# Kernel optimization log

Measured on AMD Instinct MI355X. Metric: run time of the kernel, lower is better.

The kernel has to match this reference:

```python
import jax, jax.numpy as jnp
import numpy as np

M, N, E, ES, D = 50000, 20000, 200000, 100000, 256

def _ln(x, g, b, eps=1e-5):
    mu = jnp.mean(x, -1, keepdims=True)
    var = jnp.mean((x - mu) ** 2, -1, keepdims=True)
    return (x - mu) * jax.lax.rsqrt(var + eps) * g + b

def _bn_train(x, g, b, eps=1e-5):
    # BatchNorm1d forward in training mode: batch statistics over rows
    mu = jnp.mean(x, 0)
    var = jnp.mean((x - mu) ** 2, 0)
    return (x - mu) * jax.lax.rsqrt(var + eps) * g + b

def _encoder(x, source, Wq, Wk, Wv, Wm, bm, ln1_g, ln1_b, mw1, mb1, mw2, mb2, ln2_g, ln2_b):
    # LoFTR-style linear-attention cross encoder, nhead=1
    Q = jax.nn.elu(x @ Wq) + 1.0          # [L,D]
    K = jax.nn.elu(source @ Wk) + 1.0     # [S,D]
    V = source @ Wv                        # [S,D]
    KV = K.T @ V                           # [D,D]
    Z = Q @ jnp.sum(K, 0) + 1e-6           # [L]
    msg = (Q @ KV) / Z[:, None]            # [L,D]
    msg = _ln(msg @ Wm + bm, ln1_g, ln1_b)
    y = jnp.concatenate([x, msg], -1)      # [L,2D]
    y = jax.nn.relu(y @ mw1 + mb1) @ mw2 + mb2
    return x + _ln(y, ln2_g, ln2_b)

def setup_inputs() -> dict:
    key = jax.random.key(0)
    ks = jax.random.split(key, 20)
    s = 1.0 / np.sqrt(D)
    s2 = 1.0 / np.sqrt(2 * D)
    inp = {
        'h_nodes': jax.random.normal(ks[0], (M, D), jnp.float32),
        's_u': jax.random.normal(ks[1], (N, D), jnp.float32),
        'g_src': jax.random.randint(ks[2], (E,), 0, M, jnp.int32),
        'g_dst': jax.random.randint(ks[3], (E,), 0, M, jnp.int32),
        's_src': jax.random.randint(ks[4], (ES,), 0, N, jnp.int32),
        's_dst': jax.random.randint(ks[5], (ES,), 0, N, jnp.int32),
        'conv_w': jax.random.normal(ks[6], (1, 2, 3), jnp.float32) * 0.3,
        'conv_b': jnp.zeros((1,), jnp.float32),
        'W2': jax.random.normal(ks[7], (D, D), jnp.float32) * s,
        'b2': jnp.zeros((D,), jnp.float32),
        'W4': jax.random.normal(ks[8], (D, D), jnp.float32) * s,
        'b4': jnp.zeros((D,), jnp.float32),
        'bn_g': jnp.ones((D,), jnp.float32),
        'bn_b': jnp.zeros((D,), jnp.float32),
        'Wq': jax.random.normal(ks[9], (D, D), jnp.float32) * s,
        'Wk': jax.random.normal(ks[10], (D, D), jnp.float32) * s,
        'Wv': jax.random.normal(ks[11], (D, D), jnp.float32) * s,
        'Wm': jax.random.normal(ks[12], (D, D), jnp.float32) * s,
        'bm': jnp.zeros((D,), jnp.float32),
        'ln1_g': jnp.ones((D,), jnp.float32),
        'ln1_b': jnp.zeros((D,), jnp.float32),
        'mw1': jax.random.normal(ks[13], (2 * D, 2 * D), jnp.float32) * s2,
        'mb1': jnp.zeros((2 * D,), jnp.float32),
        'mw2': jax.random.normal(ks[14], (2 * D, D), jnp.float32) * s2,
        'mb2': jnp.zeros((D,), jnp.float32),
        'ln2_g': jnp.ones((D,), jnp.float32),
        'ln2_b': jnp.zeros((D,), jnp.float32),
    }
    return inp

def reference(h_nodes, s_u, g_src, g_dst, s_src, s_dst, conv_w, conv_b, W2, b2, W4, b4,
              bn_g, bn_b, Wq, Wk, Wv, Wm, bm, ln1_g, ln1_b, mw1, mb1, mw2, mb2, ln2_g, ln2_b):
    enc = lambda x, src: _encoder(x, src, Wq, Wk, Wv, Wm, bm, ln1_g, ln1_b,
                                  mw1, mb1, mw2, mb2, ln2_g, ln2_b)
    # --- local edge features: gather src/dst, Conv1d(2->1,k=3,p=1), Linear ---
    src = h_nodes[g_src]                         # [E,D]
    dst = h_nodes[g_dst]                         # [E,D]
    edge_in = jnp.stack([src, dst], 1)           # [E,2,D]
    xp = jnp.pad(edge_in, ((0, 0), (0, 0), (1, 1)))
    conv = conv_b[0]
    for c in range(2):
        for j in range(3):
            conv = conv + conv_w[0, c, j] * xp[:, c, j:j + D]
    lr_e_local = conv @ W2 + b2                  # [E,D]
    # --- CrossTransformer (shared encoder weights across HUR/UVR/UUR) ---
    x = enc(h_nodes[:N], s_u)                    # user refinement [N,D]
    h_n = h_nodes.at[:N].set(x)
    edge = enc(h_n[g_src], h_n[g_dst])           # [E,D]
    social_edge = enc(x[s_src], x[s_dst])        # [ES,D]
    # --- fuse + BN + ReLU (dropout off for deterministic reference) ---
    lr_e = edge @ W4 + b4 + lr_e_local
    lr_e = jax.nn.relu(_bn_train(lr_e, bn_g, bn_b))
    social_edge = _bn_train(social_edge, bn_g, bn_b)
    return (lr_e, social_edge)
```

## Files before the change

### kernel.cpp

```cpp
#include <hip/hip_runtime.h>

static constexpr int Mn  = 50000;
static constexpr int Nn  = 20000;
static constexpr int En  = 200000;
static constexpr int ESn = 100000;

typedef short short8v __attribute__((ext_vector_type(8)));
typedef short short4v __attribute__((ext_vector_type(4)));
typedef float f32x4   __attribute__((ext_vector_type(4)));

__device__ __forceinline__ float b2f(unsigned short h) {
  unsigned int u = ((unsigned int)h) << 16;
  return __builtin_bit_cast(float, u);
}
__device__ __forceinline__ unsigned short f2b(float f) {
  unsigned int u = __builtin_bit_cast(unsigned int, f);
  u = (u + 0x7FFFu + ((u >> 16) & 1u)) >> 16;
  return (unsigned short)u;
}
__device__ __forceinline__ void gld16(const void* g, void* l) {
  __builtin_amdgcn_global_load_lds(
      (const __attribute__((address_space(1))) void*)g,
      (__attribute__((address_space(3))) void*)l, 16, 0, 0);
}

__global__ __launch_bounds__(256) void cvt_b(const float* __restrict__ s,
                                             unsigned short* __restrict__ d, long n) {
  long g  = (long)blockIdx.x*256 + threadIdx.x;
  long st = (long)gridDim.x*256;
  for (; g*8 < n; g += st) {
    const float4 a = *(const float4*)(s + g*8);
    const float4 b = *(const float4*)(s + g*8 + 4);
    short8v o;
    o[0]=(short)f2b(a.x); o[1]=(short)f2b(a.y); o[2]=(short)f2b(a.z); o[3]=(short)f2b(a.w);
    o[4]=(short)f2b(b.x); o[5]=(short)f2b(b.y); o[6]=(short)f2b(b.z); o[7]=(short)f2b(b.w);
    *(short8v*)(d + g*8) = o;
  }
}

__global__ __launch_bounds__(128) void wp_build(const float* __restrict__ W, int K, int N,
    unsigned short* __restrict__ WP, int KKd, int kg0) {
  const int t = threadIdx.x;
  const int kk2 = t >> 6, l = t & 63;
  const int c16 = blockIdx.x, ky = blockIdx.y;
  const int k0 = ky*64 + kk2*32 + (l>>4)*8;
  const int n  = c16*16 + (l&15);
  short8v o;
#pragma unroll
  for (int e=0;e<8;++e) o[e] = (short)f2b(W[(long)(k0+e)*N + n]);
  *(short8v*)(WP + (((long)c16*KKd + kg0 + ky*2+kk2)*64 + l)*8) = o;
}

__global__ __launch_bounds__(256) void kvw_mul(const float* __restrict__ KV,
    const float* __restrict__ Wm, float* __restrict__ KVW) {
  const int a = blockIdx.x;
  const int c = threadIdx.x;
  float s = 0.f;
  for (int b = 0; b < 256; ++b) s += KV[a*256 + b] * Wm[(long)b*256 + c];
  KVW[a*256 + c] = s;
}

__global__ __launch_bounds__(256) void count_idx(const int* __restrict__ idx, int n,
                                                 int* __restrict__ cnt) {
  int i = blockIdx.x*256 + threadIdx.x;
  const int st = gridDim.x*256;
  for (; i < n; i += st) atomicAdd(&cnt[idx[i]], 1);
}

__global__ __launch_bounds__(256,3) void gemm_kv(
    const unsigned short* __restrict__ X, int aoff,
    const unsigned short* __restrict__ WkP, const unsigned short* __restrict__ WvP,
    unsigned short* __restrict__ KbT, unsigned short* __restrict__ VbT,
    float* __restrict__ pS, int ldp, int nrows, const int* __restrict__ cntw)
{
  __shared__ short xb[4][64*64];
  const int t = threadIdx.x;
  const int w = t >> 6, l = t & 63, q = l >> 4, hw = l & 15;
  const int r0 = blockIdx.x << 6;

  {
    const int sr = l >> 3, sc = l & 7;
    const int gcol = ((sc ^ sr) << 3);
#pragma unroll
    for (int j=0;j<2;++j) {
      int lr = r0 + j*32 + w*8 + sr;
      int lrc = lr < nrows ? lr : nrows-1;
      const unsigned short* src = X + (long)(aoff+lrc)*256 + gcol;
#pragma unroll
      for (int ks=0;ks<4;++ks)
        gld16(src + ks*64, &xb[ks][(j*32 + w*8)*64]);
    }
  }
  asm volatile("s_waitcnt vmcnt(0)" ::: "memory");
  __builtin_amdgcn_s_barrier();

#pragma unroll
  for (int pass=0; pass<2; ++pass) {
    const unsigned short* WP = pass ? WvP : WkP;
    unsigned short* O = pass ? VbT : KbT;
    f32x4 acc[4][4];
#pragma unroll
    for (int m=0;m<4;++m)
#pragma unroll
      for (int n=0;n<4;++n) acc[m][n] = (f32x4){0.f,0.f,0.f,0.f};
    short8v bfc[4], bfn[4];
#pragma unroll
    for (int n=0;n<4;++n)
      bfc[n] = *(const short8v*)(WP + (((long)(w*4+n)*8)*64 + l)*8);
#pragma unroll
    for (int st=0; st<8; ++st) {
      if (st < 7) {
#pragma unroll
        for (int n=0;n<4;++n)
          bfn[n] = *(const short8v*)(WP + (((long)(w*4+n)*8 + st+1)*64 + l)*8);
      }
      const int ks = st >> 1;
      const int kc = ((st&1)<<2) + q;
      short8v af[4];
#pragma unroll
      for (int m=0;m<4;++m)
        af[m] = *(const short8v*)&xb[ks][(m*16+hw)*64 + ((kc^(hw&7))<<3)];
      __builtin_amdgcn_s_setprio(1);
#pragma unroll
      for (int m=0;m<4;++m)
#pragma unroll
        for (int n=0;n<4;++n)
          acc[m][n] = __builtin_amdgcn_mfma_f32_16x16x32_bf16(af[m], bfc[n], acc[m][n], 0,0,0);
      __builtin_amdgcn_s_setprio(0);
#pragma unroll
      for (int n=0;n<4;++n) bfc[n] = bfn[n];
    }
    float colsum[4] = {0.f,0.f,0.f,0.f};
#pragma unroll
    for (int m=0;m<4;++m)
#pragma unroll
      for (int n=0;n<4;++n) {
        const int c = w*64 + n*16 + hw;
        short4v o4;
#pragma unroll
        for (int i=0;i<4;++i) {
          const int lr = r0 + m*16 + q*4 + i;
          float v = 0.f;
          if (lr < nrows) {
            v = acc[m][n][i];
            if (pass == 0) {
              v = v > 0.f ? v + 1.f : __expf(v);
              if (cntw) v *= (float)cntw[aoff + lr];
            }
          }
          if (pass == 0) colsum[n] += v;
          o4[i] = (short)f2b(v);
        }
        *(short4v*)(O + (long)c*ldp + r0 + m*16 + q*4) = o4;
      }
    if (pass == 0) {
#pragma unroll
      for (int n=0;n<4;++n) {
        float s = colsum[n];
        s += __shfl_xor(s, 16);
        s += __shfl_xor(s, 32);
        if (q == 0) pS[(long)blockIdx.x*256 + w*64 + n*16 + hw] = s;
      }
    }
  }
}

__global__ __launch_bounds__(256) void ksum_red(const float* __restrict__ pS, int nb,
    float* __restrict__ Ks) {
  __shared__ float ws[4];
  const int c = blockIdx.x;
  const int t = threadIdx.x;
  float s = 0.f;
  for (int b = t; b < nb; b += 256) s += pS[(long)b*256 + c];
#pragma unroll
  for (int off=32; off; off>>=1) s += __shfl_xor(s, off);
  if ((t & 63) == 0) ws[t >> 6] = s;
  __syncthreads();
  if (t == 0) Ks[c] += ws[0] + ws[1] + ws[2] + ws[3];
}

__global__ __launch_bounds__(256,4) void ktv_mfma(
    const unsigned short* __restrict__ KbT, const unsigned short* __restrict__ VbT,
    int ldp, int rpp, float* __restrict__ pKV)
{
  const int t  = threadIdx.x;
  const int w  = t >> 6;
  const int l  = t & 63;
  const int q  = l >> 4;
  const int hw = l & 15;
  const int wa = w >> 1, wb = w & 1;
  const int a0 = blockIdx.x << 7;
  const int b0 = blockIdx.y << 7;
  const int rbeg = blockIdx.z * rpp;
  const int rend = min(ldp, rbeg + rpp);

  f32x4 acc[4][4];
#pragma unroll
  for (int m=0;m<4;++m)
#pragma unroll
    for (int n=0;n<4;++n) acc[m][n] = (f32x4){0.f,0.f,0.f,0.f};

  const unsigned short* ap[4];
  const unsigned short* bp[4];
#pragma unroll
  for (int m=0;m<4;++m) ap[m] = KbT + (long)(a0 + wa*64 + m*16 + hw)*ldp + q*8;
#pragma unroll
  for (int n=0;n<4;++n) bp[n] = VbT + (long)(b0 + wb*64 + n*16 + hw)*ldp + q*8;

#pragma unroll 4
  for (int r = rbeg; r < rend; r += 32) {
    short8v af[4], bf[4];
#pragma unroll
    for (int m=0;m<4;++m) af[m] = *(const short8v*)(ap[m] + r);
#pragma unroll
    for (int n=0;n<4;++n) bf[n] = *(const short8v*)(bp[n] + r);
#pragma unroll
    for (int m=0;m<4;++m)
#pragma unroll
      for (int n=0;n<4;++n)
        acc[m][n] = __builtin_amdgcn_mfma_f32_16x16x32_bf16(af[m], bf[n], acc[m][n], 0,0,0);
  }

  const long base = (long)blockIdx.z * 65536;
#pragma unroll
  for (int m=0;m<4;++m)
#pragma unroll
    for (int i=0;i<4;++i) {
      const int a = a0 + wa*64 + m*16 + q*4 + i;
#pragma unroll
      for (int n=0;n<4;++n) {
        const int b = b0 + wb*64 + n*16 + hw;
        pKV[base + (long)a*256 + b] = acc[m][n][i];
      }
    }
}

__global__ __launch_bounds__(256) void kv_accum(const float* __restrict__ pKV, int P,
                                                float* __restrict__ KV) {
  const int i = blockIdx.x*256 + threadIdx.x;
  float s = 0.f;
  for (int p=0;p<P;++p) s += pKV[(long)p*65536 + i];
  KV[i] += s;
}

template<int OMODE>
__global__ __launch_bounds__(256,2) void encB(
    const unsigned short* __restrict__ X, int aoff,
    const unsigned short* __restrict__ WqP, const unsigned short* __restrict__ KVWP,
    const unsigned short* __restrict__ m1P, const unsigned short* __restrict__ m2P,
    const float* __restrict__ Ksum, const float* __restrict__ bmv,
    const float* __restrict__ l1g, const float* __restrict__ l1b,
    const float* __restrict__ mb1, const float* __restrict__ mb2,
    const float* __restrict__ l2g, const float* __restrict__ l2b,
    const unsigned short* __restrict__ WfP,
    void* outv, int dc0, int nrows)
{
  __shared__ short xb[4][64*64];
  __shared__ short qb[4][64*64];
  __shared__ short y1b[64*64];
  __shared__ float2 red[64][4];
  __shared__ float Zl[64];

  const int t = threadIdx.x;
  const int w = t >> 6, l = t & 63, q = l >> 4, hw = l & 15;
  const int wc = w;
  const int r0 = blockIdx.x << 6;
  const int sr = l >> 3, sc = l & 7;
  const int gcol = ((sc ^ sr) << 3);

  {
#pragma unroll
    for (int j=0;j<2;++j) {
      int lr = r0 + j*32 + w*8 + sr;
      int lrc = lr < nrows ? lr : nrows-1;
      const unsigned short* src = X + (long)(aoff+lrc)*256 + gcol;
#pragma unroll
      for (int ks=0;ks<4;++ks)
        gld16(src + ks*64, &xb[ks][(j*32 + w*8)*64]);
    }
  }
  asm volatile("s_waitcnt vmcnt(0)" ::: "memory");
  __builtin_amdgcn_s_barrier();

  f32x4 acc[4][4];

  auto GEMM256 = [&](const short* Asrc, const unsigned short* WP) {
#pragma unroll
    for (int m=0;m<4;++m)
#pragma unroll
      for (int n=0;n<4;++n) acc[m][n] = (f32x4){0.f,0.f,0.f,0.f};
    short8v bfc[4], bfn[4];
#pragma unroll
    for (int n=0;n<4;++n)
      bfc[n] = *(const short8v*)(WP + (((long)(wc*4+n)*8)*64 + l)*8);
#pragma unroll
    for (int st=0; st<8; ++st) {
      if (st < 7) {
#pragma unroll
        for (int n=0;n<4;++n)
          bfn[n] = *(const short8v*)(WP + (((long)(wc*4+n)*8 + st+1)*64 + l)*8);
      }
      const int ks = st >> 1;
      const int kc = ((st&1)<<2) + q;
      short8v af[4];
#pragma unroll
      for (int m=0;m<4;++m)
        af[m] = *(const short8v*)&Asrc[ks*4096 + (m*16+hw)*64 + ((kc^(hw&7))<<3)];
      __builtin_amdgcn_s_setprio(1);
#pragma unroll
      for (int m=0;m<4;++m)
#pragma unroll
        for (int n=0;n<4;++n)
          acc[m][n] = __builtin_amdgcn_mfma_f32_16x16x32_bf16(af[m], bfc[n], acc[m][n], 0,0,0);
      __builtin_amdgcn_s_setprio(0);
#pragma unroll
      for (int n=0;n<4;++n) bfc[n] = bfn[n];
    }
  };

  GEMM256(&xb[0][0], WqP);
  {
    float ksv[4];
#pragma unroll
    for (int n=0;n<4;++n) ksv[n] = Ksum[wc*64+n*16+hw];
#pragma unroll
    for (int m=0;m<4;++m)
#pragma unroll
      for (int n=0;n<4;++n)
#pragma unroll
        for (int i=0;i<4;++i) {
          float v = acc[m][n][i];
          acc[m][n][i] = v > 0.f ? v + 1.f : __expf(v);
        }
#pragma unroll
    for (int m=0;m<4;++m)
#pragma unroll
      for (int i=0;i<4;++i) {
        float z = 0.f;
#pragma unroll
        for (int n=0;n<4;++n) z += acc[m][n][i]*ksv[n];
#pragma unroll
        for (int off=1; off<16; off<<=1) z += __shfl_xor(z, off);
        if (hw==0) red[m*16+q*4+i][wc] = make_float2(z, 0.f);
      }
#pragma unroll
    for (int m=0;m<4;++m)
#pragma unroll
      for (int i=0;i<4;++i) {
        const int row = m*16+q*4+i;
        const int sw = row & 7;
#pragma unroll
        for (int n=0;n<4;++n)
          qb[wc][row*64 + (((n*2+(hw>>3)) ^ sw)<<3) + (hw&7)] = (short)f2b(acc[m][n][i]);
      }
  }
  __syncthreads();
  if (wc==0 && hw==0) {
#pragma unroll
    for (int m=0;m<4;++m)
#pragma unroll
      for (int i=0;i<4;++i) {
        const int row = m*16+q*4+i;
        Zl[row] = red[row][0].x + red[row][1].x + red[row][2].x + red[row][3].x + 1e-6f;
      }
  }

  GEMM256(&qb[0][0], KVWP);
  __syncthreads();
#pragma unroll
  for (int m=0;m<4;++m) {
    const f32x4 z = *(const f32x4*)&Zl[m*16+q*4];
#pragma unroll
    for (int i=0;i<4;++i) {
      const float iz = 1.f / z[i];
#pragma unroll
      for (int n=0;n<4;++n) acc[m][n][i] *= iz;
    }
  }
  {
    float lg[4], lb[4];
#pragma unroll
    for (int n=0;n<4;++n) {
      const int c = wc*64+n*16+hw;
      const float bv = bmv[c];
      lg[n] = l1g[c]; lb[n] = l1b[c];
#pragma unroll
      for (int m=0;m<4;++m)
#pragma unroll
        for (int i=0;i<4;++i) acc[m][n][i] += bv;
    }
    float s1[4][4], s2[4][4];
#pragma unroll
    for (int m=0;m<4;++m)
#pragma unroll
      for (int i=0;i<4;++i) {
        float s=0.f, sq=0.f;
#pragma unroll
        for (int n=0;n<4;++n){ const float v=acc[m][n][i]; s+=v; sq+=v*v; }
        s1[m][i]=s; s2[m][i]=sq;
      }
#pragma unroll
    for (int off=1; off<16; off<<=1)
#pragma unroll
      for (int m=0;m<4;++m)
#pragma unroll
        for (int i=0;i<4;++i) {
          s1[m][i] += __shfl_xor(s1[m][i], off);
          s2[m][i] += __shfl_xor(s2[m][i], off);
        }
    if (hw==0) {
#pragma unroll
      for (int m=0;m<4;++m)
#pragma unroll
        for (int i=0;i<4;++i)
          red[m*16+q*4+i][wc] = make_float2(s1[m][i], s2[m][i]);
    }
    __syncthreads();
#pragma unroll
    for (int m=0;m<4;++m)
#pragma unroll
      for (int i=0;i<4;++i) {
        const int row = m*16+q*4+i;
        float ts=0.f, tq=0.f;
#pragma unroll
        for (int ww=0;ww<4;++ww){ const float2 v=red[row][ww]; ts+=v.x; tq+=v.y; }
        const float mmu = ts*(1.f/256.f);
        float var = tq*(1.f/256.f) - mmu*mmu;
        var = var>0.f ? var : 0.f;
        const float rs = rsqrtf(var + 1e-5f);
        const int sw = row & 7;
#pragma unroll
        for (int n=0;n<4;++n) {
          const float v = (acc[m][n][i]-mmu)*rs*lg[n] + lb[n];
          qb[wc][row*64 + (((n*2+(hw>>3)) ^ sw)<<3) + (hw&7)] = (short)f2b(v);
        }
      }
  }
  __syncthreads();

  f32x4 oacc[4][4];
#pragma unroll
  for (int m=0;m<4;++m)
#pragma unroll
    for (int n=0;n<4;++n) oacc[m][n] = (f32x4){0.f,0.f,0.f,0.f};

  for (int ct=0; ct<8; ++ct) {
    f32x4 ya[4];
#pragma unroll
    for (int m=0;m<4;++m) ya[m] = (f32x4){0.f,0.f,0.f,0.f};
    {
      short8v b0c, b0n;
      b0c = *(const short8v*)(m1P + (((long)(ct*4+wc)*16)*64 + l)*8);
#pragma unroll
      for (int st=0; st<16; ++st) {
        if (st < 15)
          b0n = *(const short8v*)(m1P + (((long)(ct*4+wc)*16 + st+1)*64 + l)*8);
        const int ks = st >> 1;
        const int kc = ((st&1)<<2) + q;
        const short* As_ = (ks<4) ? &xb[ks][0] : &qb[ks-4][0];
        __builtin_amdgcn_s_setprio(1);
#pragma unroll
        for (int m=0;m<4;++m) {
          const short8v af = *(const short8v*)&As_[(m*16+hw)*64 + ((kc^(hw&7))<<3)];
          ya[m] = __builtin_amdgcn_mfma_f32_16x16x32_bf16(af, b0c, ya[m], 0,0,0);
        }
        __builtin_amdgcn_s_setprio(0);
        b0c = b0n;
      }
    }
    const float b1 = mb1[ct*64 + wc*16 + hw];
#pragma unroll
    for (int m=0;m<4;++m)
#pragma unroll
      for (int i=0;i<4;++i) {
        const int row = m*16+q*4+i;
        float v = ya[m][i] + b1; v = v>0.f ? v : 0.f;
        y1b[row*64 + (((wc*2+(hw>>3)) ^ (row&7))<<3) + (hw&7)] = (short)f2b(v);
      }
    __syncthreads();
    {
      short8v bfc[4], bfn[4];
#pragma unroll
      for (int n=0;n<4;++n)
        bfc[n] = *(const short8v*)(m2P + (((long)(wc*4+n)*16 + ct*2)*64 + l)*8);
#pragma unroll
      for (int kk=0;kk<2;++kk) {
        if (kk == 0) {
#pragma unroll
          for (int n=0;n<4;++n)
            bfn[n] = *(const short8v*)(m2P + (((long)(wc*4+n)*16 + ct*2+1)*64 + l)*8);
        }
        const int kc = (kk<<2)+q;
        short8v af[4];
#pragma unroll
        for (int m=0;m<4;++m)
          af[m] = *(const short8v*)&y1b[(m*16+hw)*64 + ((kc^(hw&7))<<3)];
        __builtin_amdgcn_s_setprio(1);
#pragma unroll
        for (int m=0;m<4;++m)
#pragma unroll
          for (int n=0;n<4;++n)
            oacc[m][n] = __builtin_amdgcn_mfma_f32_16x16x32_bf16(af[m], bfc[n], oacc[m][n], 0,0,0);
        __builtin_amdgcn_s_setprio(0);
#pragma unroll
        for (int n=0;n<4;++n) bfc[n] = bfn[n];
      }
    }
    __syncthreads();
  }

  {
    float lg[4], lb[4];
#pragma unroll
    for (int n=0;n<4;++n) {
      const int c = wc*64+n*16+hw;
      const float bv = mb2[c];
      lg[n] = l2g[c]; lb[n] = l2b[c];
#pragma unroll
      for (int m=0;m<4;++m)
#pragma unroll
        for (int i=0;i<4;++i) oacc[m][n][i] += bv;
    }
    float s1[4][4], s2[4][4];
#pragma unroll
    for (int m=0;m<4;++m)
#pragma unroll
      for (int i=0;i<4;++i) {
        float s=0.f, sq=0.f;
#pragma unroll
        for (int n=0;n<4;++n){ const float v=oacc[m][n][i]; s+=v; sq+=v*v; }
        s1[m][i]=s; s2[m][i]=sq;
      }
#pragma unroll
    for (int off=1; off<16; off<<=1)
#pragma unroll
      for (int m=0;m<4;++m)
#pragma unroll
        for (int i=0;i<4;++i) {
          s1[m][i] += __shfl_xor(s1[m][i], off);
          s2[m][i] += __shfl_xor(s2[m][i], off);
        }
    if (hw==0) {
#pragma unroll
      for (int m=0;m<4;++m)
#pragma unroll
        for (int i=0;i<4;++i)
          red[m*16+q*4+i][wc] = make_float2(s1[m][i], s2[m][i]);
    }
    __syncthreads();
#pragma unroll
    for (int m=0;m<4;++m)
#pragma unroll
      for (int i=0;i<4;++i) {
        const int row = m*16+q*4+i;
        const int lr = r0 + row;
        if (lr >= nrows) continue;
        float ts=0.f, tq=0.f;
#pragma unroll
        for (int ww=0;ww<4;++ww){ const float2 v=red[row][ww]; ts+=v.x; tq+=v.y; }
        const float mmu = ts*(1.f/256.f);
        float var = tq*(1.f/256.f) - mmu*mmu;
        var = var>0.f ? var : 0.f;
        const float rs = rsqrtf(var + 1e-5f);
        const int sw = row & 7;
#pragma unroll
        for (int n=0;n<4;++n) {
          const int c = wc*64+n*16+hw;
          float v = (oacc[m][n][i]-mmu)*rs*lg[n] + lb[n];
          v += b2f((unsigned short)xb[wc][row*64 + (((n*2+(hw>>3)) ^ sw)<<3) + (hw&7)]);
          if constexpr (OMODE == 2) {
            qb[wc][row*64 + (((n*2+(hw>>3)) ^ sw)<<3) + (hw&7)] = (short)f2b(v);
          } else {
            const long off2 = (long)(dc0+lr)*256 + c;
            if constexpr (OMODE == 1) ((float*)outv)[off2] = v;
            else ((unsigned short*)outv)[off2] = f2b(v);
          }
        }
      }
  }

  if constexpr (OMODE == 2) {
    __syncthreads();
    GEMM256(&qb[0][0], WfP);
#pragma unroll
    for (int m=0;m<4;++m)
#pragma unroll
      for (int i=0;i<4;++i) {
        const int lr = r0 + m*16 + q*4 + i;
        if (lr >= nrows) continue;
#pragma unroll
        for (int n=0;n<4;++n)
          ((float*)outv)[(long)(dc0+lr)*256 + wc*64+n*16+hw] = acc[m][n][i];
      }
  }
}

__global__ __launch_bounds__(256,3) void edge_final(
    const float* __restrict__ h, const int* __restrict__ gs, const int* __restrict__ gd,
    const float* __restrict__ cw, const float* __restrict__ cb,
    const unsigned short* __restrict__ W2P, const float* __restrict__ EW4,
    const float* __restrict__ b4, const float* __restrict__ b2,
    float* __restrict__ lr_e, int nrows)
{
  __shared__ short xb[4][64*64];
  const int t = threadIdx.x;
  const int w = t >> 6, l = t & 63, q = l >> 4, hw = l & 15;
  const int r0 = blockIdx.x << 6;

  const float c0=cw[0],c1=cw[1],c2=cw[2],c3=cw[3],c4=cw[4],c5=cw[5],cbb=cb[0];
  for (int it=0; it<16; ++it) {
    const int row = w*16 + it;
    const int lr = r0 + row;
    const int lrc = lr < nrows ? lr : nrows-1;
    const float4 s = *(const float4*)(h + (long)gs[lrc]*256 + l*4);
    const float4 d = *(const float4*)(h + (long)gd[lrc]*256 + l*4);
    float smw = __shfl_up(s.w, 1); if (l==0) smw = 0.f;
    float spx = __shfl_down(s.x, 1); if (l==63) spx = 0.f;
    float dmw = __shfl_up(d.w, 1); if (l==0) dmw = 0.f;
    float dpx = __shfl_down(d.x, 1); if (l==63) dpx = 0.f;
    short4v o;
    o[0]=(short)f2b(cbb + c0*smw + c1*s.x + c2*s.y + c3*dmw + c4*d.x + c5*d.y);
    o[1]=(short)f2b(cbb + c0*s.x + c1*s.y + c2*s.z + c3*d.x + c4*d.y + c5*d.z);
    o[2]=(short)f2b(cbb + c0*s.y + c1*s.z + c2*s.w + c3*d.y + c4*d.z + c5*d.w);
    o[3]=(short)f2b(cbb + c0*s.z + c1*s.w + c2*spx + c3*d.z + c4*d.w + c5*dpx);
    const int ks = l >> 4;
    const int g  = (l & 15) >> 1;
    *(short4v*)&xb[ks][row*64 + ((g ^ (row&7))<<3) + (l&1)*4] = o;
  }
  __syncthreads();

  f32x4 acc[4][4];
#pragma unroll
  for (int m=0;m<4;++m)
#pragma unroll
    for (int n=0;n<4;++n) acc[m][n] = (f32x4){0.f,0.f,0.f,0.f};
  short8v bfc[4], bfn[4];
#pragma unroll
  for (int n=0;n<4;++n)
    bfc[n] = *(const short8v*)(W2P + (((long)(w*4+n)*8)*64 + l)*8);
#pragma unroll
  for (int st=0; st<8; ++st) {
    if (st < 7) {
#pragma unroll
      for (int n=0;n<4;++n)
        bfn[n] = *(const short8v*)(W2P + (((long)(w*4+n)*8 + st+1)*64 + l)*8);
    }
    const int ks = st >> 1;
    const int kc = ((st&1)<<2) + q;
    short8v af[4];
#pragma unroll
    for (int m=0;m<4;++m)
      af[m] = *(const short8v*)&xb[ks][(m*16+hw)*64 + ((kc^(hw&7))<<3)];
    __builtin_amdgcn_s_setprio(1);
#pragma unroll
    for (int m=0;m<4;++m)
#pragma unroll
      for (int n=0;n<4;++n)
        acc[m][n] = __builtin_amdgcn_mfma_f32_16x16x32_bf16(af[m], bfc[n], acc[m][n], 0,0,0);
    __builtin_amdgcn_s_setprio(0);
#pragma unroll
    for (int n=0;n<4;++n) bfc[n] = bfn[n];
  }
  float bia[4];
#pragma unroll
  for (int n=0;n<4;++n) {
    const int c = w*64+n*16+hw;
    bia[n] = b4[c] + b2[c];
  }
#pragma unroll
  for (int m=0;m<4;++m)
#pragma unroll
    for (int i=0;i<4;++i) {
      const int lr = r0 + m*16 + q*4 + i;
      if (lr >= nrows) continue;
      const long rid = (long)gs[lr];
#pragma unroll
      for (int n=0;n<4;++n) {
        const int c = w*64+n*16+hw;
        lr_e[(long)lr*256 + c] = acc[m][n][i] + EW4[rid*256 + c] + bia[n];
      }
    }
}

__global__ __launch_bounds__(256) void bn_stats(const float* __restrict__ X, long rows,
    int rpb, float* __restrict__ part) {
  const int p = blockIdx.x, w = threadIdx.x>>6, l = threadIdx.x&63;
  long r = (long)p*rpb + w;
  long r1 = (long)(p+1)*rpb; if (r1 > rows) r1 = rows;
  f32x4 s = (f32x4){0,0,0,0}, s2 = (f32x4){0,0,0,0};
  for (; r < r1; r += 4) {
    const float4 v = *(const float4*)(X + r*256 + l*4);
    s[0]+=v.x; s[1]+=v.y; s[2]+=v.z; s[3]+=v.w;
    s2[0]+=v.x*v.x; s2[1]+=v.y*v.y; s2[2]+=v.z*v.z; s2[3]+=v.w*v.w;
  }
  const long pe = (long)p*4 + w;
  *(f32x4*)&part[pe*512 + l*4] = s;
  *(f32x4*)&part[pe*512 + 256 + l*4] = s2;
}

__global__ __launch_bounds__(256) void bnw_stats(const float* __restrict__ X,
    const int* __restrict__ cnt, int rows, float* __restrict__ part) {
  const int b = blockIdx.x, c = threadIdx.x;
  float s=0.f, s2=0.f;
  for (int r=b; r<rows; r+=64) {
    const float wgt = (float)cnt[r];
    if (wgt != 0.f) {
      const float v = X[(long)r*256 + c];
      s += wgt*v; s2 += wgt*v*v;
    }
  }
  part[(long)b*512 + c] = s;
  part[(long)b*512 + 256 + c] = s2;
}

__global__ __launch_bounds__(256) void bn_mid(const float* __restrict__ part, int PE,
    float* __restrict__ mid) {
  const int g = blockIdx.x, c = threadIdx.x;
  float s=0.f, s2=0.f;
  for (int p=g; p<PE; p+=64) {
    s  += part[(long)p*512 + c];
    s2 += part[(long)p*512 + 256 + c];
  }
  mid[(long)g*512 + c] = s;
  mid[(long)g*512 + 256 + c] = s2;
}

__global__ __launch_bounds__(256) void bn_finalize(const float* __restrict__ part, int P,
    long rows, const float* __restrict__ g, const float* __restrict__ b,
    float* __restrict__ scale, float* __restrict__ shift) {
  const int c = threadIdx.x;
  float s=0.f, s2=0.f;
  for (int p=0;p<P;++p) { s += part[(long)p*512 + c]; s2 += part[(long)p*512 + 256 + c]; }
  const float inv = 1.f/(float)rows;
  const float mu = s*inv;
  float var = s2*inv - mu*mu;
  var = var > 0.f ? var : 0.f;
  const float rs = rsqrtf(var + 1e-5f);
  scale[c] = g[c]*rs;
  shift[c] = b[c] - mu*g[c]*rs;
}

template<bool R>
__global__ __launch_bounds__(256) void bn_apply(float* __restrict__ X, long rows,
    const float* __restrict__ sc, const float* __restrict__ sh) {
  const long n4 = rows*64;
  long i = (long)blockIdx.x*256 + threadIdx.x;
  const long st = (long)gridDim.x*256;
  for (; i<n4; i+=st) {
    const int cq = (int)(i & 63);
    float4 v = ((float4*)X)[i];
    const float4 s4 = ((const float4*)sc)[cq];
    const float4 h4 = ((const float4*)sh)[cq];
    v.x = v.x*s4.x + h4.x; v.y = v.y*s4.y + h4.y;
    v.z = v.z*s4.z + h4.z; v.w = v.w*s4.w + h4.w;
    if (R) { v.x=fmaxf(v.x,0.f); v.y=fmaxf(v.y,0.f); v.z=fmaxf(v.z,0.f); v.w=fmaxf(v.w,0.f); }
    ((float4*)X)[i] = v;
  }
}

__global__ __launch_bounds__(256) void bn_apply_gather(const float* __restrict__ nodeS,
    const int* __restrict__ sidx, long rows,
    const float* __restrict__ sc, const float* __restrict__ sh,
    float* __restrict__ out) {
  const long n4 = rows*64;
  long i = (long)blockIdx.x*256 + threadIdx.x;
  const long st = (long)gridDim.x*256;
  for (; i<n4; i+=st) {
    const long row = i >> 6;
    const int cq = (int)(i & 63);
    const long rid = (long)sidx[row];
    float4 v = *(const float4*)(nodeS + rid*256 + cq*4);
    const float4 s4 = ((const float4*)sc)[cq];
    const float4 h4 = ((const float4*)sh)[cq];
    v.x = v.x*s4.x + h4.x; v.y = v.y*s4.y + h4.y;
    v.z = v.z*s4.z + h4.z; v.w = v.w*s4.w + h4.w;
    ((float4*)out)[i] = v;
  }
}

struct Ctx {
  const unsigned short *WkP,*WvP,*WqP,*m1P,*m2P;
  unsigned short* KVWP;
  const float *Wm;
  float* KVW;
  const float *bm,*l1g,*l1b,*mb1,*mb2,*l2g,*l2b;
  unsigned short *bufA,*bufB;
  float *pKV,*pS,*KV;
  long CH;
  hipStream_t st;
};

static void phaseA(const Ctx& c, long S, const unsigned short* Bsrc, const int* cnt) {
  hipMemsetAsync(c.KV, 0, 65792*sizeof(float), c.st);
  for (long s0=0; s0<S; s0+=c.CH) {
    const int n = (int)((S-s0 < c.CH) ? (S-s0) : c.CH);
    const int gb = (n+63)/64;
    const int ldp = gb*64;
    gemm_kv<<<gb,256,0,c.st>>>(Bsrc, (int)s0, c.WkP, c.WvP, c.bufA, c.bufB, c.pS, ldp, n, cnt);
    const int P = (ldp+511)/512;
    ktv_mfma<<<dim3(2,2,P),256,0,c.st>>>(c.bufA, c.bufB, ldp, 512, c.pKV);
    kv_accum<<<256,256,0,c.st>>>(c.pKV, P, c.KV);
    ksum_red<<<256,256,0,c.st>>>(c.pS, gb, c.KV+65536);
  }
  kvw_mul<<<256,256,0,c.st>>>(c.KV, c.Wm, c.KVW);
  wp_build<<<dim3(16,4),128,0,c.st>>>(c.KVW, 256, 256, c.KVWP, 8, 0);
}

template<int OMODE>
static void phaseB(const Ctx& c, long L, const unsigned short* Asrc, void* out,
                   const unsigned short* WfP) {
  const float* Ksum = c.KV + 65536;
  for (long l0=0; l0<L; l0+=c.CH) {
    const int n = (int)((L-l0 < c.CH) ? (L-l0) : c.CH);
    const int gb = (n+63)/64;
    encB<OMODE><<<gb,256,0,c.st>>>(Asrc, (int)l0,
        c.WqP, c.KVWP, c.m1P, c.m2P, Ksum, c.bm, c.l1g, c.l1b,
        c.mb1, c.mb2, c.l2g, c.l2b, WfP, out, (int)l0, n);
  }
}

extern "C" void kernel_launch(void* const* d_in, const int* in_sizes, int n_in,
                              void* d_out, int out_size, void* d_ws, size_t ws_size,
                              hipStream_t stream) {
  const float* h_nodes = (const float*)d_in[0];
  const float* s_u     = (const float*)d_in[1];
  const int*   g_src   = (const int*)d_in[2];
  const int*   g_dst   = (const int*)d_in[3];
  const int*   s_src   = (const int*)d_in[4];
  const int*   s_dst   = (const int*)d_in[5];
  const float* conv_w  = (const float*)d_in[6];
  const float* conv_b  = (const float*)d_in[7];
  const float* W2      = (const float*)d_in[8];
  const float* b2      = (const float*)d_in[9];
  const float* W4      = (const float*)d_in[10];
  const float* b4      = (const float*)d_in[11];
  const float* bn_g    = (const float*)d_in[12];
  const float* bn_b    = (const float*)d_in[13];
  const float* Wq      = (const float*)d_in[14];
  const float* Wk      = (const float*)d_in[15];
  const float* Wv      = (const float*)d_in[16];
  const float* Wm      = (const float*)d_in[17];
  const float* bm      = (const float*)d_in[18];
  const float* l1g     = (const float*)d_in[19];
  const float* l1b     = (const float*)d_in[20];
  const float* mw1     = (const float*)d_in[21];
  const float* mb1     = (const float*)d_in[22];
  const float* mw2     = (const float*)d_in[23];
  const float* mb2     = (const float*)d_in[24];
  const float* l2g     = (const float*)d_in[25];
  const float* l2b     = (const float*)d_in[26];
  (void)in_sizes; (void)n_in; (void)out_size;

  float* lr_e = (float*)d_out;
  float* soc  = lr_e + (size_t)En*256;

  char* base = (char*)d_ws;
  size_t off = 0;
  auto carve = [&](size_t bytes)->void* {
    void* p = (void*)(base + off);
    off = (off + bytes + 255) & ~(size_t)255;
    return p;
  };
  unsigned short* h_nb = (unsigned short*)carve((size_t)Mn*256*2);
  unsigned short* s_ub = (unsigned short*)carve((size_t)Nn*256*2);
  unsigned short* WkP  = (unsigned short*)carve(65536*2);
  unsigned short* WvP  = (unsigned short*)carve(65536*2);
  unsigned short* WqP  = (unsigned short*)carve(65536*2);
  unsigned short* m1P  = (unsigned short*)carve(262144*2);
  unsigned short* m2P  = (unsigned short*)carve(131072*2);
  unsigned short* W4P  = (unsigned short*)carve(65536*2);
  unsigned short* W2P  = (unsigned short*)carve(65536*2);
  unsigned short* KVWP = (unsigned short*)carve(65536*2);
  float* KV            = (float*)carve(65792*4);
  float* KVW           = (float*)carve(65536*4);
  float* bnpart        = (float*)carve((size_t)2048*512*4);
  float* bnmid         = (float*)carve((size_t)64*512*4);
  float* bnscale       = (float*)carve(256*4);
  float* bnshift       = (float*)carve(256*4);
  float* EW4           = (float*)carve((size_t)Mn*256*4);
  float* nodeS         = (float*)carve((size_t)Nn*256*4);
  int* cntg            = (int*)carve((size_t)Mn*4);
  int* cnts            = (int*)carve((size_t)Nn*4);
  int* cntss           = (int*)carve((size_t)Nn*4);

  const size_t remain = ws_size > off ? ws_size - off : 0;
  long CH = (long)(remain / 1589248) * 1024;
  if (CH > 65536) CH = 65536;
  if (CH < 2048)  CH = 2048;
  unsigned short* bufA = (unsigned short*)carve((size_t)CH*256*2);
  unsigned short* bufB = (unsigned short*)carve((size_t)CH*256*2);
  float* pKV           = (float*)carve((size_t)((CH+511)/512)*65536*4);
  float* pS            = (float*)carve((size_t)(CH/64)*256*4);

  cvt_b<<<2048,256,0,stream>>>(h_nodes, h_nb, (long)Mn*256);
  cvt_b<<<1024,256,0,stream>>>(s_u, s_ub, (long)Nn*256);
  wp_build<<<dim3(16,4),128,0,stream>>>(Wk, 256,256, WkP, 8, 0);
  wp_build<<<dim3(16,4),128,0,stream>>>(Wv, 256,256, WvP, 8, 0);
  wp_build<<<dim3(16,4),128,0,stream>>>(Wq, 256,256, WqP, 8, 0);
  wp_build<<<dim3(32,8),128,0,stream>>>(mw1, 512,512, m1P, 16, 0);
  wp_build<<<dim3(16,8),128,0,stream>>>(mw2, 512,256, m2P, 16, 0);
  wp_build<<<dim3(16,4),128,0,stream>>>(W4, 256,256, W4P, 8, 0);
  wp_build<<<dim3(16,4),128,0,stream>>>(W2, 256,256, W2P, 8, 0);
  hipMemsetAsync(cntg, 0, (size_t)Mn*4, stream);
  hipMemsetAsync(cnts, 0, (size_t)Nn*4, stream);
  hipMemsetAsync(cntss,0, (size_t)Nn*4, stream);
  count_idx<<<512,256,0,stream>>>(g_dst, En, cntg);
  count_idx<<<512,256,0,stream>>>(s_dst, ESn, cnts);
  count_idx<<<512,256,0,stream>>>(s_src, ESn, cntss);

  Ctx c;
  c.WkP=WkP; c.WvP=WvP; c.WqP=WqP; c.m1P=m1P; c.m2P=m2P;
  c.KVWP=KVWP; c.Wm=Wm; c.KVW=KVW;
  c.bm=bm; c.l1g=l1g; c.l1b=l1b; c.mb1=mb1; c.mb2=mb2; c.l2g=l2g; c.l2b=l2b;
  c.bufA=bufA; c.bufB=bufB;
  c.pKV=pKV; c.pS=pS; c.KV=KV;
  c.CH=CH; c.st=stream;

  phaseA(c, Nn, s_ub, nullptr);
  phaseB<0>(c, Nn, h_nb, h_nb, nullptr);

  phaseA(c, Mn, h_nb, cntg);
  phaseB<2>(c, Mn, h_nb, EW4, W4P);
  edge_final<<<(En+63)/64,256,0,stream>>>(h_nodes, g_src, g_dst, conv_w, conv_b,
                                          W2P, EW4, b4, b2, lr_e, En);

  phaseA(c, Nn, h_nb, cnts);
  phaseB<1>(c, Nn, h_nb, nodeS, nullptr);
  bnw_stats<<<64,256,0,stream>>>(nodeS, cntss, Nn, bnmid);
  bn_finalize<<<1,256,0,stream>>>(bnmid, 64, (long)ESn, bn_g, bn_b, bnscale, bnshift);
  bn_apply_gather<<<2048,256,0,stream>>>(nodeS, s_src, (long)ESn, bnscale, bnshift, soc);

  {
    const int P3 = (En+511)/512;
    bn_stats<<<P3,256,0,stream>>>(lr_e,(long)En,512,bnpart);
    bn_mid<<<64,256,0,stream>>>(bnpart, P3*4, bnmid);
    bn_finalize<<<1,256,0,stream>>>(bnmid,64,(long)En,bn_g,bn_b,bnscale,bnshift);
    bn_apply<true><<<2048,256,0,stream>>>(lr_e,(long)En,bnscale,bnshift);
  }
}
```

Measured before the change: 1.207 ms.

## Fuse BN statistics into edge_final and stage edge output in bf16

edge_final now gathers node rows from a bf16 copy of h_nodes, computes per-block column sums and sums of squares in its epilogue, and writes a bf16 intermediate instead of fp32. This removes the separate bn_stats pass and halves the intermediate traffic. A new apply kernel reads the bf16 buffer, applies scale, shift and ReLU, and writes fp32 lr_e. Launch bounds go up to 5 blocks per CU. In exchange it adds an extra cvt pass and buffers, and rounds lr_e and the conv inputs to bf16, which costs precision.

```diff
diff --git a/kernel.cpp b/kernel.cpp
--- a/kernel.cpp
+++ b/kernel.cpp
@@ -595,12 +595,13 @@
   }
 }
 
-__global__ __launch_bounds__(256,3) void edge_final(
-    const float* __restrict__ h, const int* __restrict__ gs, const int* __restrict__ gd,
+__global__ __launch_bounds__(256,5) void edge_final(
+    const unsigned short* __restrict__ hb0, const int* __restrict__ gs,
+    const int* __restrict__ gd,
     const float* __restrict__ cw, const float* __restrict__ cb,
     const unsigned short* __restrict__ W2P, const float* __restrict__ EW4,
     const float* __restrict__ b4, const float* __restrict__ b2,
-    float* __restrict__ lr_e, int nrows)
+    unsigned short* __restrict__ lr_s, float* __restrict__ pstat, int nrows)
 {
   __shared__ short xb[4][64*64];
   const int t = threadIdx.x;
@@ -612,8 +613,13 @@
     const int row = w*16 + it;
     const int lr = r0 + row;
     const int lrc = lr < nrows ? lr : nrows-1;
-    const float4 s = *(const float4*)(h + (long)gs[lrc]*256 + l*4);
-    const float4 d = *(const float4*)(h + (long)gd[lrc]*256 + l*4);
+    const short4v sv = *(const short4v*)(hb0 + (long)gs[lrc]*256 + l*4);
+    const short4v dv = *(const short4v*)(hb0 + (long)gd[lrc]*256 + l*4);
+    float4 s, d;
+    s.x=b2f((unsigned short)sv[0]); s.y=b2f((unsigned short)sv[1]);
+    s.z=b2f((unsigned short)sv[2]); s.w=b2f((unsigned short)sv[3]);
+    d.x=b2f((unsigned short)dv[0]); d.y=b2f((unsigned short)dv[1]);
+    d.z=b2f((unsigned short)dv[2]); d.w=b2f((unsigned short)dv[3]);
     float smw = __shfl_up(s.w, 1); if (l==0) smw = 0.f;
     float spx = __shfl_down(s.x, 1); if (l==63) spx = 0.f;
     float dmw = __shfl_up(d.w, 1); if (l==0) dmw = 0.f;
@@ -667,6 +673,8 @@
     const int c = w*64+n*16+hw;
     bia[n] = b4[c] + b2[c];
   }
+  float cs[4] = {0.f,0.f,0.f,0.f};
+  float cq2[4] = {0.f,0.f,0.f,0.f};
 #pragma unroll
   for (int m=0;m<4;++m)
 #pragma unroll
@@ -677,25 +685,51 @@
 #pragma unroll
       for (int n=0;n<4;++n) {
         const int c = w*64+n*16+hw;
-        lr_e[(long)lr*256 + c] = acc[m][n][i] + EW4[rid*256 + c] + bia[n];
-      }
-    }
-}
-
-__global__ __launch_bounds__(256) void bn_stats(const float* __restrict__ X, long rows,
-    int rpb, float* __restrict__ part) {
-  const int p = blockIdx.x, w = threadIdx.x>>6, l = threadIdx.x&63;
-  long r = (long)p*rpb + w;
-  long r1 = (long)(p+1)*rpb; if (r1 > rows) r1 = rows;
-  f32x4 s = (f32x4){0,0,0,0}, s2 = (f32x4){0,0,0,0};
-  for (; r < r1; r += 4) {
-    const float4 v = *(const float4*)(X + r*256 + l*4);
-    s[0]+=v.x; s[1]+=v.y; s[2]+=v.z; s[3]+=v.w;
-    s2[0]+=v.x*v.x; s2[1]+=v.y*v.y; s2[2]+=v.z*v.z; s2[3]+=v.w*v.w;
-  }
-  const long pe = (long)p*4 + w;
-  *(f32x4*)&part[pe*512 + l*4] = s;
-  *(f32x4*)&part[pe*512 + 256 + l*4] = s2;
+        const float v = acc[m][n][i] + EW4[rid*256 + c] + bia[n];
+        cs[n] += v; cq2[n] += v*v;
+        lr_s[(long)lr*256 + c] = f2b(v);
+      }
+    }
+#pragma unroll
+  for (int n=0;n<4;++n) {
+    float a = cs[n];
+    a += __shfl_xor(a, 16);
+    a += __shfl_xor(a, 32);
+    float b = cq2[n];
+    b += __shfl_xor(b, 16);
+    b += __shfl_xor(b, 32);
+    if (q == 0) {
+      const int c = w*64+n*16+hw;
+      pstat[(long)blockIdx.x*512 + c] = a;
+      pstat[(long)blockIdx.x*512 + 256 + c] = b;
+    }
+  }
+}
+
+__global__ __launch_bounds__(256) void bn_apply_relu_cvt(
+    const unsigned short* __restrict__ Xs, long rows,
+    const float* __restrict__ sc, const float* __restrict__ sh,
+    float* __restrict__ out) {
+  const long n8 = rows*32;
+  long i = (long)blockIdx.x*256 + threadIdx.x;
+  const long st = (long)gridDim.x*256;
+  for (; i<n8; i+=st) {
+    const int cq = (int)(i & 31);
+    const short8v x = *(const short8v*)(Xs + i*8);
+    const float4 sa = ((const float4*)sc)[cq*2], sb = ((const float4*)sc)[cq*2+1];
+    const float4 ha = ((const float4*)sh)[cq*2], hb4 = ((const float4*)sh)[cq*2+1];
+    float4 o1, o2;
+    o1.x = fmaxf(b2f((unsigned short)x[0])*sa.x + ha.x, 0.f);
+    o1.y = fmaxf(b2f((unsigned short)x[1])*sa.y + ha.y, 0.f);
+    o1.z = fmaxf(b2f((unsigned short)x[2])*sa.z + ha.z, 0.f);
+    o1.w = fmaxf(b2f((unsigned short)x[3])*sa.w + ha.w, 0.f);
+    o2.x = fmaxf(b2f((unsigned short)x[4])*sb.x + hb4.x, 0.f);
+    o2.y = fmaxf(b2f((unsigned short)x[5])*sb.y + hb4.y, 0.f);
+    o2.z = fmaxf(b2f((unsigned short)x[6])*sb.z + hb4.z, 0.f);
+    o2.w = fmaxf(b2f((unsigned short)x[7])*sb.w + hb4.w, 0.f);
+    *(float4*)(out + i*8)     = o1;
+    *(float4*)(out + i*8 + 4) = o2;
+  }
 }
 
 __global__ __launch_bounds__(256) void bnw_stats(const float* __restrict__ X,
@@ -738,24 +772,6 @@
   const float rs = rsqrtf(var + 1e-5f);
   scale[c] = g[c]*rs;
   shift[c] = b[c] - mu*g[c]*rs;
-}
-
-template<bool R>
-__global__ __launch_bounds__(256) void bn_apply(float* __restrict__ X, long rows,
-    const float* __restrict__ sc, const float* __restrict__ sh) {
-  const long n4 = rows*64;
-  long i = (long)blockIdx.x*256 + threadIdx.x;
-  const long st = (long)gridDim.x*256;
-  for (; i<n4; i+=st) {
-    const int cq = (int)(i & 63);
-    float4 v = ((float4*)X)[i];
-    const float4 s4 = ((const float4*)sc)[cq];
-    const float4 h4 = ((const float4*)sh)[cq];
-    v.x = v.x*s4.x + h4.x; v.y = v.y*s4.y + h4.y;
-    v.z = v.z*s4.z + h4.z; v.w = v.w*s4.w + h4.w;
-    if (R) { v.x=fmaxf(v.x,0.f); v.y=fmaxf(v.y,0.f); v.z=fmaxf(v.z,0.f); v.w=fmaxf(v.w,0.f); }
-    ((float4*)X)[i] = v;
-  }
 }
 
 __global__ __launch_bounds__(256) void bn_apply_gather(const float* __restrict__ nodeS,
@@ -861,8 +877,9 @@
     off = (off + bytes + 255) & ~(size_t)255;
     return p;
   };
-  unsigned short* h_nb = (unsigned short*)carve((size_t)Mn*256*2);
-  unsigned short* s_ub = (unsigned short*)carve((size_t)Nn*256*2);
+  unsigned short* h_nb  = (unsigned short*)carve((size_t)Mn*256*2);
+  unsigned short* h_nb0 = (unsigned short*)carve((size_t)Mn*256*2);
+  unsigned short* s_ub  = (unsigned short*)carve((size_t)Nn*256*2);
   unsigned short* WkP  = (unsigned short*)carve(65536*2);
   unsigned short* WvP  = (unsigned short*)carve(65536*2);
   unsigned short* WqP  = (unsigned short*)carve(65536*2);
@@ -873,12 +890,13 @@
   unsigned short* KVWP = (unsigned short*)carve(65536*2);
   float* KV            = (float*)carve(65792*4);
   float* KVW           = (float*)carve(65536*4);
-  float* bnpart        = (float*)carve((size_t)2048*512*4);
+  float* bnpart        = (float*)carve((size_t)3200*512*4);
   float* bnmid         = (float*)carve((size_t)64*512*4);
   float* bnscale       = (float*)carve(256*4);
   float* bnshift       = (float*)carve(256*4);
   float* EW4           = (float*)carve((size_t)Mn*256*4);
   float* nodeS         = (float*)carve((size_t)Nn*256*4);
+  unsigned short* lr_s = (unsigned short*)carve((size_t)En*256*2);
   int* cntg            = (int*)carve((size_t)Mn*4);
   int* cnts            = (int*)carve((size_t)Nn*4);
   int* cntss           = (int*)carve((size_t)Nn*4);
@@ -893,6 +911,7 @@
   float* pS            = (float*)carve((size_t)(CH/64)*256*4);
 
   cvt_b<<<2048,256,0,stream>>>(h_nodes, h_nb, (long)Mn*256);
+  cvt_b<<<2048,256,0,stream>>>(h_nodes, h_nb0, (long)Mn*256);
   cvt_b<<<1024,256,0,stream>>>(s_u, s_ub, (long)Nn*256);
   wp_build<<<dim3(16,4),128,0,stream>>>(Wk, 256,256, WkP, 8, 0);
   wp_build<<<dim3(16,4),128,0,stream>>>(Wv, 256,256, WvP, 8, 0);
@@ -921,20 +940,18 @@
 
   phaseA(c, Mn, h_nb, cntg);
   phaseB<2>(c, Mn, h_nb, EW4, W4P);
-  edge_final<<<(En+63)/64,256,0,stream>>>(h_nodes, g_src, g_dst, conv_w, conv_b,
-                                          W2P, EW4, b4, b2, lr_e, En);
+  {
+    const int gbE = (En+63)/64;
+    edge_final<<<gbE,256,0,stream>>>(h_nb0, g_src, g_dst, conv_w, conv_b,
+                                     W2P, EW4, b4, b2, lr_s, bnpart, En);
+    bn_mid<<<64,256,0,stream>>>(bnpart, gbE, bnmid);
+    bn_finalize<<<1,256,0,stream>>>(bnmid, 64, (long)En, bn_g, bn_b, bnscale, bnshift);
+    bn_apply_relu_cvt<<<2048,256,0,stream>>>(lr_s, (long)En, bnscale, bnshift, lr_e);
+  }
 
   phaseA(c, Nn, h_nb, cnts);
   phaseB<1>(c, Nn, h_nb, nodeS, nullptr);
   bnw_stats<<<64,256,0,stream>>>(nodeS, cntss, Nn, bnmid);
   bn_finalize<<<1,256,0,stream>>>(bnmid, 64, (long)ESn, bn_g, bn_b, bnscale, bnshift);
   bn_apply_gather<<<2048,256,0,stream>>>(nodeS, s_src, (long)ESn, bnscale, bnshift, soc);
-
-  {
-    const int P3 = (En+511)/512;
-    bn_stats<<<P3,256,0,stream>>>(lr_e,(long)En,512,bnpart);
-    bn_mid<<<64,256,0,stream>>>(bnpart, P3*4, bnmid);
-    bn_finalize<<<1,256,0,stream>>>(bnmid,64,(long)En,bn_g,bn_b,bnscale,bnshift);
-    bn_apply<true><<<2048,256,0,stream>>>(lr_e,(long)En,bnscale,bnshift);
-  }
-}
+}
```

Result: slower. 1.297 ms (+7.4%).
